# Performance work log

Hardware: AMD Instinct MI355X
Metric: run time of the kernel (lower is better)

The kernel has to match this reference:

```python
import jax, jax.numpy as jnp
import numpy as np
from jax import lax

WINDOW_SIZE = 11
SIGMA = 1.5
RGB_RANGE = 1.0
K1, K2 = 0.01, 0.03
CHANNELS = 3


def gaussian_window(window_size, sigma, channels, dtype=jnp.float32):
    coords = jnp.arange(window_size, dtype=dtype) - window_size // 2
    g = jnp.exp(-(coords ** 2) / (2.0 * sigma * sigma))
    g = g / g.sum()
    w2d = jnp.outer(g, g)
    w2d = w2d / w2d.sum()
    # depthwise kernel: (C, 1, ws, ws) in OIHW with feature_group_count=C
    return jnp.broadcast_to(w2d, (channels, 1, window_size, window_size)).astype(dtype)


def _dwconv(inp, window, padding):
    # depthwise conv2d, groups = C
    C = inp.shape[1]
    return lax.conv_general_dilated(
        inp, window,
        window_strides=(1, 1),
        padding=[(padding, padding), (padding, padding)],
        feature_group_count=C,
        dimension_numbers=('NCHW', 'OIHW', 'NCHW'))


def setup_inputs() -> dict:
    key = jax.random.key(0)
    kx, ky = jax.random.split(key)
    B, C, H, W = 16, CHANNELS, 512, 512
    x = jax.random.uniform(kx, (B, C, H, W), dtype=jnp.float32)
    y = jax.random.uniform(ky, (B, C, H, W), dtype=jnp.float32)
    window = gaussian_window(WINDOW_SIZE, SIGMA, C)
    return {"x": x, "y": y, "window": window}


def reference(x, y, window):
    padding = WINDOW_SIZE // 2
    mu_x = _dwconv(x, window, padding)
    mu_y = _dwconv(y, window, padding)
    mu_x2 = mu_x * mu_x
    mu_y2 = mu_y * mu_y
    mu_xy = mu_x * mu_y
    sigma_x2 = _dwconv(x * x, window, padding) - mu_x2
    sigma_y2 = _dwconv(y * y, window, padding) - mu_y2
    sigma_xy = _dwconv(x * y, window, padding) - mu_xy
    L = RGB_RANGE
    C1 = (K1 * L) ** 2
    C2 = (K2 * L) ** 2
    ssim_map = ((2.0 * mu_xy + C1) * (2.0 * sigma_xy + C2)) / (
        (mu_x2 + mu_y2 + C1) * (sigma_x2 + sigma_y2 + C2) + 1e-12)
    loss = 1.0 - ssim_map
    return loss.mean()
```

## Files before the change

kernel.cpp:

```cpp
#include <hip/hip_runtime.h>


typedef __fp16 f16x8 __attribute__((ext_vector_type(8)));
typedef float f32x4 __attribute__((ext_vector_type(4)));
typedef unsigned u32x2 __attribute__((ext_vector_type(2)));
typedef unsigned u32x4 __attribute__((ext_vector_type(4)));

__device__ __forceinline__ unsigned pk2(float a, float b) {
    return __builtin_bit_cast(unsigned, __builtin_amdgcn_cvt_pkrtz(a, b));
}
__device__ __forceinline__ f32x4 mfma16(f16x8 a, f16x8 b, f32x4 c) {
    return __builtin_amdgcn_mfma_f32_16x16x32_f16(a, b, c, 0, 0, 0);
}
__device__ __forceinline__ f16x8 ld8(const unsigned* p) {
    const u32x2 a = *(const u32x2*)p;
    const u32x2 b = *(const u32x2*)(p + 2);
    const u32x4 w = {a.x, a.y, b.x, b.y};
    return __builtin_bit_cast(f16x8, w);
}

#define SXW 22
#define HPW 34

__global__ __launch_bounds__(256, 4) void ssim_main(
    const float* __restrict__ xg, const float* __restrict__ yg,
    const float* __restrict__ w2d, float* __restrict__ part)
{
    __shared__ __align__(16) unsigned sx[74 * SXW];
    __shared__ __align__(16) unsigned sy[74 * SXW];
    __shared__ __align__(16) unsigned hq[5][37 * HPW];
    __shared__ float gsf[12];
    __shared__ float wred[4];

    const int tid = threadIdx.x;

    if (tid < 12) {
        float s = 0.0f;
        if (tid < 11) {
            #pragma unroll
            for (int j = 0; j < 11; ++j) s += w2d[tid * 11 + j];
        }
        gsf[tid] = s;
    }

    const int x0 = blockIdx.x * 32 - 6;
    const int y0 = blockIdx.y * 64 - 5;
    const size_t zoff = (size_t)blockIdx.z * (512 * 512);
    const float* __restrict__ xp = xg + zoff;
    const float* __restrict__ yp = yg + zoff;

    const bool interior = (x0 >= 0) & (x0 + 43 < 512) & (y0 >= 0) & (y0 + 73 < 512);
    if (interior) {
        for (int it = tid; it < 74 * SXW; it += 256) {
            const int r = it / SXW, cw = it - r * SXW;
            const int o = (y0 + r) * 512 + x0 + 2 * cw;
            const float2 vx = *(const float2*)&xp[o];
            const float2 vy = *(const float2*)&yp[o];
            sx[it] = pk2(vx.x, vx.y);
            sy[it] = pk2(vy.x, vy.y);
        }
    } else {
        for (int it = tid; it < 74 * SXW; it += 256) {
            const int r = it / SXW, cw = it - r * SXW;
            const int gr = y0 + r, gc = x0 + 2 * cw;
            float xv0 = 0.f, xv1 = 0.f, yv0 = 0.f, yv1 = 0.f;
            if ((unsigned)gr < 512u) {
                const int o = gr * 512 + gc;
                if ((unsigned)gc < 512u)       { xv0 = xp[o];     yv0 = yp[o]; }
                if ((unsigned)(gc + 1) < 512u) { xv1 = xp[o + 1]; yv1 = yp[o + 1]; }
            }
            sx[it] = pk2(xv0, xv1);
            sy[it] = pk2(yv0, yv1);
        }
    }
    __syncthreads();

    const int lane = tid & 63, wv = tid >> 6;
    const int lm = lane & 15, lg = lane >> 4;

    float ssum = 0.0f;
    #pragma unroll
    for (int k = 0; k < 11; ++k)
        if (k != 5) ssum += (float)(__fp16)gsf[k];
    const __fp16 cc = (__fp16)(1.0f - ssum);
    auto tap = [&](int t) -> __fp16 {
        const unsigned u = ((unsigned)t <= 11u) ? (unsigned)t : 11u;
        const __fp16 hv = (__fp16)gsf[u];
        return (t == 5) ? cc : hv;
    };

    f16x8 bt0, bt1, afr;
    const int dd = (wv == 3) ? -6 : 0;
    #pragma unroll
    for (int e = 0; e < 8; ++e) {
        const int k = 8 * lg + e;
        bt0[e] = tap(k - lm - 1);
        bt1[e] = tap(k - lm - 5);
        afr[e] = tap(k - lm + dd);
    }

    for (int i = wv; i < 10; i += 4) {
        const int b = i >> 1, tl = i & 1;
        const int rb = (b == 4) ? 58 : 16 * b;
        const int sbase = (rb + lm) * SXW + 6 * tl + 4 * lg;
        const f16x8 xa = ld8(&sx[sbase]);
        const f16x8 ya = ld8(&sy[sbase]);
        const f16x8 bt = tl ? bt1 : bt0;
        const f32x4 z4 = {0.f, 0.f, 0.f, 0.f};
        const f32x4 dmx = mfma16(xa, bt, z4);
        const f32x4 dmy = mfma16(ya, bt, z4);
        const f32x4 dxx = mfma16(xa * xa, bt, z4);
        const f32x4 dyy = mfma16(ya * ya, bt, z4);
        const f32x4 dxy = mfma16(xa * ya, bt, z4);
        const int rp0 = (rb >> 1) + 2 * lg;
        const int col = lm + 16 * tl;
        hq[0][rp0 * HPW + col]       = pk2(dmx[0], dmx[1]);
        hq[0][(rp0 + 1) * HPW + col] = pk2(dmx[2], dmx[3]);
        hq[1][rp0 * HPW + col]       = pk2(dmy[0], dmy[1]);
        hq[1][(rp0 + 1) * HPW + col] = pk2(dmy[2], dmy[3]);
        hq[2][rp0 * HPW + col]       = pk2(dxx[0], dxx[1]);
        hq[2][(rp0 + 1) * HPW + col] = pk2(dxx[2], dxx[3]);
        hq[3][rp0 * HPW + col]       = pk2(dyy[0], dyy[1]);
        hq[3][(rp0 + 1) * HPW + col] = pk2(dyy[2], dyy[3]);
        hq[4][rp0 * HPW + col]       = pk2(dxy[0], dxy[1]);
        hq[4][(rp0 + 1) * HPW + col] = pk2(dxy[2], dxy[3]);
    }
    __syncthreads();

    f32x4 acc[2][5];
    #pragma unroll
    for (int ch = 0; ch < 2; ++ch)
        #pragma unroll
        for (int q = 0; q < 5; ++q)
            acc[ch][q] = (f32x4){0.f, 0.f, 0.f, 0.f};

    const int rpb = (wv == 3) ? 21 : 8 * wv;
    #pragma unroll
    for (int ch = 0; ch < 2; ++ch) {
        const int cb = (rpb + 4 * lg) * HPW + lm + 16 * ch;
        #pragma unroll
        for (int q = 0; q < 5; ++q) {
            const unsigned* hp = hq[q];
            const u32x4 w4 = {hp[cb], hp[cb + HPW],
                              hp[cb + 2 * HPW], hp[cb + 3 * HPW]};
            acc[ch][q] = mfma16(afr, __builtin_bit_cast(f16x8, w4), acc[ch][q]);
        }
    }

    float lsum = 0.0f;
    const float C1 = 1e-4f, C2 = 9e-4f;
    #pragma unroll
    for (int ch = 0; ch < 2; ++ch) {
        #pragma unroll
        for (int r = 0; r < 4; ++r) {
            const float mx = acc[ch][0][r], my = acc[ch][1][r];
            const float exx = acc[ch][2][r], eyy = acc[ch][3][r];
            const float exy = acc[ch][4][r];
            const float mx2 = mx * mx, my2 = my * my, mxy = mx * my;
            const float vx = exx - mx2, vy = eyy - my2, vxy = exy - mxy;
            const float num = (2.0f * mxy + C1) * (2.0f * vxy + C2);
            const float den = (mx2 + my2 + C1) * (vx + vy + C2) + 1e-12f;
            lsum = fmaf(num, __builtin_amdgcn_rcpf(den), lsum);
        }
    }

    #pragma unroll
    for (int off = 32; off > 0; off >>= 1)
        lsum += __shfl_down(lsum, off, 64);
    if ((tid & 63) == 0) wred[tid >> 6] = lsum;
    __syncthreads();
    if (tid == 0) {
        const int bid = (blockIdx.z * gridDim.y + blockIdx.y) * gridDim.x
                        + blockIdx.x;
        part[bid] = wred[0] + wred[1] + wred[2] + wred[3];
    }
}

__global__ __launch_bounds__(256) void ssim_reduce(
    const float* __restrict__ part, float* __restrict__ out,
    int n, float invN)
{
    __shared__ float wred[4];
    float s = 0.0f;
    for (int i = threadIdx.x; i < n; i += 256) s += part[i];
    #pragma unroll
    for (int off = 32; off > 0; off >>= 1)
        s += __shfl_down(s, off, 64);
    if ((threadIdx.x & 63) == 0) wred[threadIdx.x >> 6] = s;
    __syncthreads();
    if (threadIdx.x == 0)
        out[0] = 1.0f - (wred[0] + wred[1] + wred[2] + wred[3]) * invN;
}

extern "C" void kernel_launch(void* const* d_in, const int* in_sizes, int n_in,
                              void* d_out, int out_size, void* d_ws, size_t ws_size,
                              hipStream_t stream) {
    const float* x   = (const float*)d_in[0];
    const float* y   = (const float*)d_in[1];
    const float* w2d = (const float*)d_in[2];
    float* out  = (float*)d_out;
    float* part = (float*)d_ws;

    const int H = 512, W = 512;
    const int total = in_sizes[0];
    const int Z = total / (H * W);

    dim3 grid(W / 32, H / 64, Z);
    const int nblocks = (W / 32) * (H / 64) * Z;
    ssim_main<<<grid, 256, 0, stream>>>(x, y, w2d, part);

    const float invN = 1.0f / (float)total;
    ssim_reduce<<<1, 256, 0, stream>>>(part, out, nblocks, invN);
}
```

Measured before the change: 163.1 us.

## Process SSIM statistics in chunks to shrink LDS and swizzle block order

The horizontal-pass buffer drops from five planes to two. The five statistics are now computed in three sequential chunks, each followed by a vertical MFMA pass, which cuts LDS use so more workgroups can be resident (launch bounds raised to 7). The row pitch changes to 33 to alter the bank mapping, and a workgroup index swizzle spreads consecutive blocks across images, likely aimed at XCD/L2 locality. In exchange the kernel needs extra barriers and reloads the input tile from LDS three times.

```diff
diff --git a/kernel.cpp b/kernel.cpp
--- a/kernel.cpp
+++ b/kernel.cpp
@@ -20,15 +20,15 @@
 }
 
 #define SXW 22
-#define HPW 34
-
-__global__ __launch_bounds__(256, 4) void ssim_main(
+#define HPW 33
+
+__global__ __launch_bounds__(256, 7) void ssim_main(
     const float* __restrict__ xg, const float* __restrict__ yg,
     const float* __restrict__ w2d, float* __restrict__ part)
 {
     __shared__ __align__(16) unsigned sx[74 * SXW];
     __shared__ __align__(16) unsigned sy[74 * SXW];
-    __shared__ __align__(16) unsigned hq[5][37 * HPW];
+    __shared__ __align__(16) unsigned hq[2][37 * HPW];
     __shared__ float gsf[12];
     __shared__ float wred[4];
 
@@ -43,9 +43,14 @@
         gsf[tid] = s;
     }
 
-    const int x0 = blockIdx.x * 32 - 6;
-    const int y0 = blockIdx.y * 64 - 5;
-    const size_t zoff = (size_t)blockIdx.z * (512 * 512);
+    const int nwg = 128 * (int)gridDim.z;
+    const int flat = (int)blockIdx.x + 16 * ((int)blockIdx.y + 8 * (int)blockIdx.z);
+    const int swz = (flat & 7) * (nwg >> 3) + (flat >> 3);
+    const int bx = swz & 15, by = (swz >> 4) & 7, bz = swz >> 7;
+
+    const int x0 = bx * 32 - 6;
+    const int y0 = by * 64 - 5;
+    const size_t zoff = (size_t)bz * (512 * 512);
     const float* __restrict__ xp = xg + zoff;
     const float* __restrict__ yp = yg + zoff;
 
@@ -99,34 +104,6 @@
         afr[e] = tap(k - lm + dd);
     }
 
-    for (int i = wv; i < 10; i += 4) {
-        const int b = i >> 1, tl = i & 1;
-        const int rb = (b == 4) ? 58 : 16 * b;
-        const int sbase = (rb + lm) * SXW + 6 * tl + 4 * lg;
-        const f16x8 xa = ld8(&sx[sbase]);
-        const f16x8 ya = ld8(&sy[sbase]);
-        const f16x8 bt = tl ? bt1 : bt0;
-        const f32x4 z4 = {0.f, 0.f, 0.f, 0.f};
-        const f32x4 dmx = mfma16(xa, bt, z4);
-        const f32x4 dmy = mfma16(ya, bt, z4);
-        const f32x4 dxx = mfma16(xa * xa, bt, z4);
-        const f32x4 dyy = mfma16(ya * ya, bt, z4);
-        const f32x4 dxy = mfma16(xa * ya, bt, z4);
-        const int rp0 = (rb >> 1) + 2 * lg;
-        const int col = lm + 16 * tl;
-        hq[0][rp0 * HPW + col]       = pk2(dmx[0], dmx[1]);
-        hq[0][(rp0 + 1) * HPW + col] = pk2(dmx[2], dmx[3]);
-        hq[1][rp0 * HPW + col]       = pk2(dmy[0], dmy[1]);
-        hq[1][(rp0 + 1) * HPW + col] = pk2(dmy[2], dmy[3]);
-        hq[2][rp0 * HPW + col]       = pk2(dxx[0], dxx[1]);
-        hq[2][(rp0 + 1) * HPW + col] = pk2(dxx[2], dxx[3]);
-        hq[3][rp0 * HPW + col]       = pk2(dyy[0], dyy[1]);
-        hq[3][(rp0 + 1) * HPW + col] = pk2(dyy[2], dyy[3]);
-        hq[4][rp0 * HPW + col]       = pk2(dxy[0], dxy[1]);
-        hq[4][(rp0 + 1) * HPW + col] = pk2(dxy[2], dxy[3]);
-    }
-    __syncthreads();
-
     f32x4 acc[2][5];
     #pragma unroll
     for (int ch = 0; ch < 2; ++ch)
@@ -135,16 +112,46 @@
             acc[ch][q] = (f32x4){0.f, 0.f, 0.f, 0.f};
 
     const int rpb = (wv == 3) ? 21 : 8 * wv;
-    #pragma unroll
-    for (int ch = 0; ch < 2; ++ch) {
-        const int cb = (rpb + 4 * lg) * HPW + lm + 16 * ch;
+
+    #pragma unroll
+    for (int chunk = 0; chunk < 3; ++chunk) {
+        for (int i = wv; i < 10; i += 4) {
+            const int b = i >> 1, tl = i & 1;
+            const int rb = (b == 4) ? 58 : 16 * b;
+            const int sbase = (rb + lm) * SXW + 6 * tl + 4 * lg;
+            const f16x8 xa = ld8(&sx[sbase]);
+            const f16x8 ya = ld8(&sy[sbase]);
+            const f16x8 bt = tl ? bt1 : bt0;
+            const f32x4 z4 = {0.f, 0.f, 0.f, 0.f};
+            f32x4 d0, d1;
+            if (chunk == 0)      { d0 = mfma16(xa, bt, z4);      d1 = mfma16(ya, bt, z4); }
+            else if (chunk == 1) { d0 = mfma16(xa * xa, bt, z4); d1 = mfma16(ya * ya, bt, z4); }
+            else                 { d0 = mfma16(xa * ya, bt, z4); }
+            const int rp0 = (rb >> 1) + 2 * lg;
+            const int col = lm + 16 * tl;
+            hq[0][rp0 * HPW + col]       = pk2(d0[0], d0[1]);
+            hq[0][(rp0 + 1) * HPW + col] = pk2(d0[2], d0[3]);
+            if (chunk < 2) {
+                hq[1][rp0 * HPW + col]       = pk2(d1[0], d1[1]);
+                hq[1][(rp0 + 1) * HPW + col] = pk2(d1[2], d1[3]);
+            }
+        }
+        __syncthreads();
+
         #pragma unroll
-        for (int q = 0; q < 5; ++q) {
-            const unsigned* hp = hq[q];
-            const u32x4 w4 = {hp[cb], hp[cb + HPW],
-                              hp[cb + 2 * HPW], hp[cb + 3 * HPW]};
-            acc[ch][q] = mfma16(afr, __builtin_bit_cast(f16x8, w4), acc[ch][q]);
-        }
+        for (int ch = 0; ch < 2; ++ch) {
+            const int cb = (rpb + 4 * lg) * HPW + lm + 16 * ch;
+            #pragma unroll
+            for (int s = 0; s < 2; ++s) {
+                if (chunk == 2 && s == 1) continue;
+                const unsigned* hp = hq[s];
+                const u32x4 w4 = {hp[cb], hp[cb + HPW],
+                                  hp[cb + 2 * HPW], hp[cb + 3 * HPW]};
+                acc[ch][2 * chunk + s] =
+                    mfma16(afr, __builtin_bit_cast(f16x8, w4), acc[ch][2 * chunk + s]);
+            }
+        }
+        if (chunk < 2) __syncthreads();
     }
 
     float lsum = 0.0f;
@@ -169,11 +176,7 @@
         lsum += __shfl_down(lsum, off, 64);
     if ((tid & 63) == 0) wred[tid >> 6] = lsum;
     __syncthreads();
-    if (tid == 0) {
-        const int bid = (blockIdx.z * gridDim.y + blockIdx.y) * gridDim.x
-                        + blockIdx.x;
-        part[bid] = wred[0] + wred[1] + wred[2] + wred[3];
-    }
+    if (tid == 0) part[swz] = wred[0] + wred[1] + wred[2] + wred[3];
 }
 
 __global__ __launch_bounds__(256) void ssim_reduce(
```

New measurement: 150.4 us. 7.8% less time.
